# Kernel optimization log

Hardware: AMD Instinct MI355X
Metric: run time of the kernel (lower is better)

Reference implementation:

```python
import jax, jax.numpy as jnp
import numpy as np

NUMERICAL_STABILIZER = 1e-3


def relu_kernel(data, projection_matrix):
    # data: [B,L,H,D], projection_matrix: [M,D] -> [B,L,H,M]
    ratio = 1.0 / jnp.sqrt(jnp.asarray(projection_matrix.shape[0], dtype=data.dtype))
    data_dash = ratio * jnp.einsum('blhd,md->blhm', data, projection_matrix)
    return jax.nn.relu(data_dash) + NUMERICAL_STABILIZER


def favor_causal(query, key, value, projection_matrix):
    # query/key/value: [B,L,H,D]; projection_matrix: [M,D]
    qp = relu_kernel(query, projection_matrix)  # [B,L,H,M]
    kp = relu_kernel(key, projection_matrix)    # [B,L,H,M]
    # move L to scan axis: [L,B,H,*]
    qs = jnp.transpose(qp, (1, 0, 2, 3))
    ks = jnp.transpose(kp, (1, 0, 2, 3))
    vs = jnp.transpose(value, (1, 0, 2, 3))

    B, H, M = qs.shape[1], qs.shape[2], qs.shape[3]
    D = vs.shape[3]
    kv0 = jnp.zeros((B, H, M, D), dtype=qs.dtype)
    ksum0 = jnp.zeros((B, H, M), dtype=qs.dtype)

    def step(carry, inp):
        kv_sum, k_sum = carry
        q_t, k_t, v_t = inp  # [B,H,M], [B,H,M], [B,H,D]
        kv_sum = kv_sum + jnp.einsum('bhm,bhd->bhmd', k_t, v_t)
        k_sum = k_sum + k_t
        num_t = jnp.einsum('bhmd,bhm->bhd', kv_sum, q_t)  # [B,H,D]
        den_t = jnp.einsum('bhm,bhm->bh', q_t, k_sum)     # [B,H]
        return (kv_sum, k_sum), (num_t, den_t)

    _, (num, den) = jax.lax.scan(step, (kv0, ksum0), (qs, ks, vs))
    # num: [L,B,H,D], den: [L,B,H]
    out = num / den[..., None]
    return jnp.transpose(out, (1, 0, 2, 3))  # [B,L,H,D]


def setup_inputs() -> dict:
    key = jax.random.key(0)
    k1, k2, k3, k4 = jax.random.split(key, 4)
    B, L, H, D, M = 2, 4096, 8, 64, 128
    return {
        'query': jax.random.normal(k1, (B, L, H, D), dtype=jnp.float32),
        'key': jax.random.normal(k2, (B, L, H, D), dtype=jnp.float32),
        'value': jax.random.normal(k3, (B, L, H, D), dtype=jnp.float32),
        'projection_matrix': jax.random.normal(k4, (M, D), dtype=jnp.float32),
    }


def reference(query, key, value, projection_matrix):
    return favor_causal(query, key, value, projection_matrix)
```

## Files before the change

kernel.cpp:

```cpp
#include <hip/hip_runtime.h>


#define B_ 2
#define L_ 4096
#define H_ 8
#define D_ 64
#define M_ 128
#define BH_ 16
#define HD_ 512
#define LHD_ (L_*HD_)
#define C_ 64
#define T_ 64
#define RATIO 0.08838834764831845f
#define EPS 1e-3f

#define REC_CS 8320
#define REC_F  8192
#define QF_OFF 8519680
#define N2_OFF 16908288
#define RS_OFF 25296896
#define P_OFF  25427968

#define VT_S  72
#define KFT_S 72
#define TM_S  136

typedef __attribute__((ext_vector_type(8))) short bf16x8;
typedef __attribute__((ext_vector_type(4))) short bf16x4;
typedef __attribute__((ext_vector_type(4))) float f32x4;

__device__ __forceinline__ short f2bf(float f) {
  union { float f; unsigned u; } x; x.f = f;
  unsigned r = (x.u + 0x7fffu + ((x.u >> 16) & 1u)) >> 16;
  return (short)r;
}
__device__ __forceinline__ float bf2f(short s) {
  union { unsigned u; float f; } x; x.u = ((unsigned)(unsigned short)s) << 16;
  return x.f;
}
__device__ __forceinline__ bf16x8 load_cvt8(const float* p) {
  float4 a = *(const float4*)p;
  float4 b = *(const float4*)(p + 4);
  union { bf16x8 v; short s[8]; } u;
  u.s[0]=f2bf(a.x); u.s[1]=f2bf(a.y); u.s[2]=f2bf(a.z); u.s[3]=f2bf(a.w);
  u.s[4]=f2bf(b.x); u.s[5]=f2bf(b.y); u.s[6]=f2bf(b.z); u.s[7]=f2bf(b.w);
  return u.v;
}
#define MFMA(a,b,c) __builtin_amdgcn_mfma_f32_16x16x32_bf16((a),(b),(c),0,0,0)

__global__ __launch_bounds__(256) void k0(
    const float* __restrict__ P, unsigned short* __restrict__ ws)
{
  const int i = (blockIdx.x*256 + threadIdx.x)*4;
  float4 p4 = *(const float4*)(P + i);
  union { bf16x4 v; short s[4]; } u;
  u.s[0]=f2bf(p4.x); u.s[1]=f2bf(p4.y); u.s[2]=f2bf(p4.z); u.s[3]=f2bf(p4.w);
  *(bf16x4*)(ws + P_OFF + i) = u.v;
}

__global__ __launch_bounds__(256) void k1(
    const float* __restrict__ qq, const float* __restrict__ kk,
    const float* __restrict__ vv, unsigned short* __restrict__ ws)
{
  __shared__ short Vt[64*VT_S];
  __shared__ short Kft[128*KFT_S];
  __shared__ short KfTM[64*TM_S];
  __shared__ short QfTM[64*TM_S];

  const int tid = threadIdx.x, bid = blockIdx.x;
  const int bh = bid >> 6, c = bid & 63;
  const int b = bh >> 3, h = bh & 7;
  const int lane = tid & 63, w = tid >> 6, quad = lane >> 4, l15 = lane & 15;
  const size_t gbase = (size_t)b*LHD_ + (size_t)h*D_;
  const int t0 = c*T_;
  const unsigned short* Pb = ws + P_OFF;

  for (int fi = tid; fi < 64*16; fi += 256) {
    int t = fi >> 4, d4 = (fi & 15)*4;
    float4 v4 = *(const float4*)(vv + gbase + (size_t)(t0+t)*HD_ + d4);
    Vt[(d4+0)*VT_S + t] = f2bf(v4.x);
    Vt[(d4+1)*VT_S + t] = f2bf(v4.y);
    Vt[(d4+2)*VT_S + t] = f2bf(v4.z);
    Vt[(d4+3)*VT_S + t] = f2bf(v4.w);
  }

  const float* qrow = qq + gbase + (size_t)(t0 + 16*w + l15)*HD_;
  const float* krow = kk + gbase + (size_t)(t0 + 16*w + l15)*HD_;
  bf16x8 bq0 = load_cvt8(qrow + quad*8);
  bf16x8 bq1 = load_cvt8(qrow + 32 + quad*8);
  bf16x8 bk0 = load_cvt8(krow + quad*8);
  bf16x8 bk1 = load_cvt8(krow + 32 + quad*8);
  #pragma unroll
  for (int ct = 0; ct < 8; ++ct) {
    bf16x8 ap0 = *(const bf16x8*)(Pb + (ct*16 + l15)*64 + quad*8);
    bf16x8 ap1 = *(const bf16x8*)(Pb + (ct*16 + l15)*64 + 32 + quad*8);
    f32x4 qa = {0.f,0.f,0.f,0.f}, ka = {0.f,0.f,0.f,0.f};
    qa = MFMA(ap0,bq0,qa); qa = MFMA(ap1,bq1,qa);
    ka = MFMA(ap0,bk0,ka); ka = MFMA(ap1,bk1,ka);
    union { bf16x4 v; short s[4]; } pq, pk;
    #pragma unroll
    for (int reg = 0; reg < 4; ++reg) {
      int m = 16*ct + 4*quad + reg;
      short qv = f2bf(fmaxf(qa[reg]*RATIO, 0.f) + EPS);
      short kv = f2bf(fmaxf(ka[reg]*RATIO, 0.f) + EPS);
      pq.s[reg] = qv; pk.s[reg] = kv;
      Kft[m*KFT_S + 16*w + l15] = kv;
    }
    *(bf16x4*)&QfTM[(16*w+l15)*TM_S + 16*ct + 4*quad] = pq.v;
    *(bf16x4*)&KfTM[(16*w+l15)*TM_S + 16*ct + 4*quad] = pk.v;
  }
  __syncthreads();

  unsigned short* csb = ws + (size_t)(bh*C_+c)*REC_CS;
  unsigned short* qfb = ws + QF_OFF + (size_t)(bh*C_+c)*REC_F;

  {
    int tt = tid >> 4, mb = (tid & 15)*8;
    #pragma unroll
    for (int j = 0; j < 4; ++j) {
      bf16x8 v8 = *(const bf16x8*)&QfTM[(tt + 16*j)*TM_S + mb];
      *(bf16x8*)(qfb + (tt + 16*j)*128 + mb) = v8;
    }
  }
  bf16x8 qfr[4];
  #pragma unroll
  for (int ks2 = 0; ks2 < 4; ++ks2)
    qfr[ks2] = *(const bf16x8*)&QfTM[(16*w+l15)*TM_S + ks2*32 + quad*8];

  if (tid < 128) {
    float s = 0.f;
    #pragma unroll
    for (int i = 0; i < 8; ++i) {
      bf16x8 r = *(const bf16x8*)&Kft[tid*KFT_S + 8*i];
      #pragma unroll
      for (int j = 0; j < 8; ++j) s += bf2f(r[j]);
    }
    csb[64*128 + tid] = (unsigned short)f2bf(s);
  }

  {
    bf16x8 av0 = *(const bf16x8*)&Vt[(16*w + l15)*VT_S + quad*8];
    bf16x8 av1 = *(const bf16x8*)&Vt[(16*w + l15)*VT_S + 32 + quad*8];
    #pragma unroll
    for (int mt = 0; mt < 8; ++mt) {
      bf16x8 b0 = *(const bf16x8*)&Kft[(16*mt + l15)*KFT_S + quad*8];
      bf16x8 b1 = *(const bf16x8*)&Kft[(16*mt + l15)*KFT_S + 32 + quad*8];
      f32x4 acc = {0.f,0.f,0.f,0.f};
      acc = MFMA(b0, av0, acc);
      acc = MFMA(b1, av1, acc);
      union { bf16x4 v; short s[4]; } pc;
      #pragma unroll
      for (int reg = 0; reg < 4; ++reg) pc.s[reg] = f2bf(acc[reg]);
      *(bf16x4*)(csb + (16*w + l15)*128 + 16*mt + 4*quad) = pc.v;
    }
  }
  __syncthreads();

  short* Sm = QfTM;

  f32x4 sacc[4];
  #pragma unroll
  for (int jt = 0; jt < 4; ++jt) { f32x4 z = {0.f,0.f,0.f,0.f}; sacc[jt] = z; }
  #pragma unroll
  for (int ks2 = 0; ks2 < 4; ++ks2) {
    #pragma unroll
    for (int jt = 0; jt < 4; ++jt) {
      bf16x8 bb = *(const bf16x8*)&KfTM[(16*jt + l15)*TM_S + ks2*32 + quad*8];
      sacc[jt] = MFMA(qfr[ks2], bb, sacc[jt]);
    }
  }
  float rs[4] = {0.f,0.f,0.f,0.f};
  #pragma unroll
  for (int jt = 0; jt < 4; ++jt)
    #pragma unroll
    for (int reg = 0; reg < 4; ++reg) {
      int row = 16*w + 4*quad + reg;
      int j = l15 + 16*jt;
      float val = (j <= row) ? sacc[jt][reg] : 0.f;
      rs[reg] += val;
      Sm[row*TM_S + j] = f2bf(val);
    }
  #pragma unroll
  for (int reg = 0; reg < 4; ++reg) {
    rs[reg] += __shfl_xor(rs[reg], 1);
    rs[reg] += __shfl_xor(rs[reg], 2);
    rs[reg] += __shfl_xor(rs[reg], 4);
    rs[reg] += __shfl_xor(rs[reg], 8);
  }
  float* rsg = (float*)(ws + RS_OFF);
  if (l15 < 4) {
    float v = (l15==0) ? rs[0] : (l15==1) ? rs[1] : (l15==2) ? rs[2] : rs[3];
    rsg[bh*L_ + t0 + 16*w + 4*quad + l15] = v;
  }

  float* n2 = (float*)(ws + N2_OFF);
  f32x4 nacc[4];
  #pragma unroll
  for (int ct = 0; ct < 4; ++ct) { f32x4 z = {0.f,0.f,0.f,0.f}; nacc[ct] = z; }
  #pragma unroll
  for (int kss = 0; kss < 2; ++kss) {
    bf16x8 sb = *(const bf16x8*)&Sm[(16*w + l15)*TM_S + kss*32 + quad*8];
    #pragma unroll
    for (int ct = 0; ct < 4; ++ct) {
      bf16x8 a = *(const bf16x8*)&Vt[(16*ct + l15)*VT_S + kss*32 + quad*8];
      nacc[ct] = MFMA(a, sb, nacc[ct]);
    }
  }
  const int tg = t0 + 16*w + l15;
  #pragma unroll
  for (int ct = 0; ct < 4; ++ct) {
    float4 o;
    o.x = nacc[ct][0]; o.y = nacc[ct][1]; o.z = nacc[ct][2]; o.w = nacc[ct][3];
    *(float4*)(n2 + gbase + (size_t)tg*HD_ + 16*ct + 4*quad) = o;
  }
}

__global__ __launch_bounds__(256) void k2(unsigned short* __restrict__ ws)
{
  const int gid = blockIdx.x*256 + threadIdx.x;
  const int bh = gid / REC_CS, e = gid % REC_CS;
  unsigned short* base = ws + (size_t)bh*C_*REC_CS + e;
  short v[64];
  #pragma unroll
  for (int c2 = 0; c2 < 64; ++c2) v[c2] = (short)base[(size_t)c2*REC_CS];
  float run = 0.f;
  #pragma unroll
  for (int c2 = 0; c2 < 64; ++c2) {
    base[(size_t)c2*REC_CS] = (unsigned short)f2bf(run);
    run += bf2f(v[c2]);
  }
}

__global__ __launch_bounds__(256) void k3(
    const unsigned short* __restrict__ ws, float* __restrict__ out)
{
  const int tid = threadIdx.x, bid = blockIdx.x;
  const int bh = bid >> 6, c = bid & 63;
  const int b = bh >> 3, h = bh & 7;
  const int lane = tid & 63, w = tid >> 6, quad = lane >> 4, l15 = lane & 15;
  const size_t gbase = (size_t)b*LHD_ + (size_t)h*D_;
  const int t0 = c*T_;
  const unsigned short* csb = ws + (size_t)(bh*C_+c)*REC_CS;
  const unsigned short* qfb = ws + QF_OFF + (size_t)(bh*C_+c)*REC_F;
  const float* n2 = (const float*)(ws + N2_OFF);
  const float* rsg = (const float*)(ws + RS_OFF);

  const int tg = t0 + 16*w + l15;

  float4 nv[4];
  #pragma unroll
  for (int ct = 0; ct < 4; ++ct)
    nv[ct] = *(const float4*)(n2 + gbase + (size_t)tg*HD_ + 16*ct + 4*quad);
  float rsv = rsg[bh*L_ + tg];

  bf16x8 qfB[4], ksf[4];
  #pragma unroll
  for (int ks2 = 0; ks2 < 4; ++ks2) {
    qfB[ks2] = *(const bf16x8*)(qfb + (16*w + l15)*128 + ks2*32 + quad*8);
    ksf[ks2] = *(const bf16x8*)(csb + 64*128 + ks2*32 + quad*8);
  }
  float dp = 0.f;
  #pragma unroll
  for (int ks2 = 0; ks2 < 4; ++ks2)
    #pragma unroll
    for (int j = 0; j < 8; ++j) dp += bf2f(qfB[ks2][j]) * bf2f(ksf[ks2][j]);
  dp += __shfl_xor(dp, 16);
  dp += __shfl_xor(dp, 32);
  float inv = 1.f / (dp + rsv);

  f32x4 nacc[4];
  #pragma unroll
  for (int ct = 0; ct < 4; ++ct) { f32x4 z = {0.f,0.f,0.f,0.f}; nacc[ct] = z; }
  #pragma unroll
  for (int ks2 = 0; ks2 < 4; ++ks2) {
    #pragma unroll
    for (int ct = 0; ct < 4; ++ct) {
      bf16x8 a = *(const bf16x8*)(csb + (16*ct + l15)*128 + ks2*32 + quad*8);
      nacc[ct] = MFMA(a, qfB[ks2], nacc[ct]);
    }
  }
  #pragma unroll
  for (int ct = 0; ct < 4; ++ct) {
    float4 o;
    o.x = (nacc[ct][0] + nv[ct].x) * inv;
    o.y = (nacc[ct][1] + nv[ct].y) * inv;
    o.z = (nacc[ct][2] + nv[ct].z) * inv;
    o.w = (nacc[ct][3] + nv[ct].w) * inv;
    *(float4*)(out + gbase + (size_t)tg*HD_ + 16*ct + 4*quad) = o;
  }
}

extern "C" void kernel_launch(void* const* d_in, const int* in_sizes, int n_in,
                              void* d_out, int out_size, void* d_ws, size_t ws_size,
                              hipStream_t stream) {
  const float* q = (const float*)d_in[0];
  const float* k = (const float*)d_in[1];
  const float* v = (const float*)d_in[2];
  const float* P = (const float*)d_in[3];
  float* out = (float*)d_out;
  unsigned short* ws = (unsigned short*)d_ws;

  dim3 blk(256);
  k0<<<dim3(8), blk, 0, stream>>>(P, ws);
  k1<<<dim3(BH_*C_), blk, 0, stream>>>(q, k, v, ws);
  k2<<<dim3(520), blk, 0, stream>>>(ws);
  k3<<<dim3(BH_*C_), blk, 0, stream>>>(ws, out);
}
```

Baseline: 133.0 us.

## Swizzle LDS layouts, vectorize chunk scan, stage chunk state in LDS

```diff
diff --git a/kernel.cpp b/kernel.cpp
--- a/kernel.cpp
+++ b/kernel.cpp
@@ -21,9 +21,8 @@
 #define RS_OFF 25296896
 #define P_OFF  25427968
 
-#define VT_S  72
-#define KFT_S 72
-#define TM_S  136
+#define SWZ64(r,c)  ((r)*64  + ((c) ^ (((r)&7)*8)))
+#define SWZ128(r,c) ((r)*128 + ((c) ^ (((r)&15)*8)))
 
 typedef __attribute__((ext_vector_type(8))) short bf16x8;
 typedef __attribute__((ext_vector_type(4))) short bf16x4;
@@ -38,9 +37,7 @@
   union { unsigned u; float f; } x; x.u = ((unsigned)(unsigned short)s) << 16;
   return x.f;
 }
-__device__ __forceinline__ bf16x8 load_cvt8(const float* p) {
-  float4 a = *(const float4*)p;
-  float4 b = *(const float4*)(p + 4);
+__device__ __forceinline__ bf16x8 cvt8(float4 a, float4 b) {
   union { bf16x8 v; short s[8]; } u;
   u.s[0]=f2bf(a.x); u.s[1]=f2bf(a.y); u.s[2]=f2bf(a.z); u.s[3]=f2bf(a.w);
   u.s[4]=f2bf(b.x); u.s[5]=f2bf(b.y); u.s[6]=f2bf(b.z); u.s[7]=f2bf(b.w);
@@ -62,10 +59,10 @@
     const float* __restrict__ qq, const float* __restrict__ kk,
     const float* __restrict__ vv, unsigned short* __restrict__ ws)
 {
-  __shared__ short Vt[64*VT_S];
-  __shared__ short Kft[128*KFT_S];
-  __shared__ short KfTM[64*TM_S];
-  __shared__ short QfTM[64*TM_S];
+  __shared__ short Vt[64*64];
+  __shared__ short Kft[128*64];
+  __shared__ short KfTM[64*128];
+  __shared__ short Scr[64*64];
 
   const int tid = threadIdx.x, bid = blockIdx.x;
   const int bh = bid >> 6, c = bid & 63;
@@ -73,23 +70,36 @@
   const int lane = tid & 63, w = tid >> 6, quad = lane >> 4, l15 = lane & 15;
   const size_t gbase = (size_t)b*LHD_ + (size_t)h*D_;
   const int t0 = c*T_;
+  const int trow = 16*w + l15;
   const unsigned short* Pb = ws + P_OFF;
+
+  const float* qrow = qq + gbase + (size_t)(t0 + trow)*HD_;
+  const float* krow = kk + gbase + (size_t)(t0 + trow)*HD_;
+  float4 q4a = *(const float4*)(qrow + quad*8);
+  float4 q4b = *(const float4*)(qrow + quad*8 + 4);
+  float4 q4c = *(const float4*)(qrow + 32 + quad*8);
+  float4 q4d = *(const float4*)(qrow + 32 + quad*8 + 4);
+  float4 k4a = *(const float4*)(krow + quad*8);
+  float4 k4b = *(const float4*)(krow + quad*8 + 4);
+  float4 k4c = *(const float4*)(krow + 32 + quad*8);
+  float4 k4d = *(const float4*)(krow + 32 + quad*8 + 4);
 
   for (int fi = tid; fi < 64*16; fi += 256) {
     int t = fi >> 4, d4 = (fi & 15)*4;
     float4 v4 = *(const float4*)(vv + gbase + (size_t)(t0+t)*HD_ + d4);
-    Vt[(d4+0)*VT_S + t] = f2bf(v4.x);
-    Vt[(d4+1)*VT_S + t] = f2bf(v4.y);
-    Vt[(d4+2)*VT_S + t] = f2bf(v4.z);
-    Vt[(d4+3)*VT_S + t] = f2bf(v4.w);
-  }
-
-  const float* qrow = qq + gbase + (size_t)(t0 + 16*w + l15)*HD_;
-  const float* krow = kk + gbase + (size_t)(t0 + 16*w + l15)*HD_;
-  bf16x8 bq0 = load_cvt8(qrow + quad*8);
-  bf16x8 bq1 = load_cvt8(qrow + 32 + quad*8);
-  bf16x8 bk0 = load_cvt8(krow + quad*8);
-  bf16x8 bk1 = load_cvt8(krow + 32 + quad*8);
+    Vt[SWZ64(d4+0, t)] = f2bf(v4.x);
+    Vt[SWZ64(d4+1, t)] = f2bf(v4.y);
+    Vt[SWZ64(d4+2, t)] = f2bf(v4.z);
+    Vt[SWZ64(d4+3, t)] = f2bf(v4.w);
+  }
+
+  bf16x8 bq0 = cvt8(q4a, q4b), bq1 = cvt8(q4c, q4d);
+  bf16x8 bk0 = cvt8(k4a, k4b), bk1 = cvt8(k4c, k4d);
+
+  unsigned short* qfb = ws + QF_OFF + (size_t)(bh*C_+c)*REC_F;
+  unsigned short* csb = ws + (size_t)(bh*C_+c)*REC_CS;
+
+  bf16x4 qreg[8];
   #pragma unroll
   for (int ct = 0; ct < 8; ++ct) {
     bf16x8 ap0 = *(const bf16x8*)(Pb + (ct*16 + l15)*64 + quad*8);
@@ -104,34 +114,29 @@
       short qv = f2bf(fmaxf(qa[reg]*RATIO, 0.f) + EPS);
       short kv = f2bf(fmaxf(ka[reg]*RATIO, 0.f) + EPS);
       pq.s[reg] = qv; pk.s[reg] = kv;
-      Kft[m*KFT_S + 16*w + l15] = kv;
-    }
-    *(bf16x4*)&QfTM[(16*w+l15)*TM_S + 16*ct + 4*quad] = pq.v;
-    *(bf16x4*)&KfTM[(16*w+l15)*TM_S + 16*ct + 4*quad] = pk.v;
+      Kft[SWZ64(m, trow)] = kv;
+    }
+    qreg[ct] = pq.v;
+    *(bf16x4*)(qfb + trow*128 + 16*ct + 4*quad) = pq.v;
+    *(bf16x4*)&KfTM[SWZ128(trow, 16*ct + 4*quad)] = pk.v;
+  }
+
+  bf16x8 qfr[4];
+  #pragma unroll
+  for (int p = 0; p < 2; ++p) {
+    #pragma unroll
+    for (int ct2 = 0; ct2 < 4; ++ct2)
+      *(bf16x4*)&Scr[SWZ64(trow, 16*ct2 + 4*quad)] = qreg[4*p + ct2];
+    qfr[2*p+0] = *(const bf16x8*)&Scr[SWZ64(trow, 8*quad)];
+    qfr[2*p+1] = *(const bf16x8*)&Scr[SWZ64(trow, 32 + 8*quad)];
   }
   __syncthreads();
-
-  unsigned short* csb = ws + (size_t)(bh*C_+c)*REC_CS;
-  unsigned short* qfb = ws + QF_OFF + (size_t)(bh*C_+c)*REC_F;
-
-  {
-    int tt = tid >> 4, mb = (tid & 15)*8;
-    #pragma unroll
-    for (int j = 0; j < 4; ++j) {
-      bf16x8 v8 = *(const bf16x8*)&QfTM[(tt + 16*j)*TM_S + mb];
-      *(bf16x8*)(qfb + (tt + 16*j)*128 + mb) = v8;
-    }
-  }
-  bf16x8 qfr[4];
-  #pragma unroll
-  for (int ks2 = 0; ks2 < 4; ++ks2)
-    qfr[ks2] = *(const bf16x8*)&QfTM[(16*w+l15)*TM_S + ks2*32 + quad*8];
 
   if (tid < 128) {
     float s = 0.f;
     #pragma unroll
     for (int i = 0; i < 8; ++i) {
-      bf16x8 r = *(const bf16x8*)&Kft[tid*KFT_S + 8*i];
+      bf16x8 r = *(const bf16x8*)&Kft[SWZ64(tid, 8*i)];
       #pragma unroll
       for (int j = 0; j < 8; ++j) s += bf2f(r[j]);
     }
@@ -139,24 +144,21 @@
   }
 
   {
-    bf16x8 av0 = *(const bf16x8*)&Vt[(16*w + l15)*VT_S + quad*8];
-    bf16x8 av1 = *(const bf16x8*)&Vt[(16*w + l15)*VT_S + 32 + quad*8];
+    bf16x8 av0 = *(const bf16x8*)&Vt[SWZ64(trow, 8*quad)];
+    bf16x8 av1 = *(const bf16x8*)&Vt[SWZ64(trow, 32 + 8*quad)];
     #pragma unroll
     for (int mt = 0; mt < 8; ++mt) {
-      bf16x8 b0 = *(const bf16x8*)&Kft[(16*mt + l15)*KFT_S + quad*8];
-      bf16x8 b1 = *(const bf16x8*)&Kft[(16*mt + l15)*KFT_S + 32 + quad*8];
+      bf16x8 b0 = *(const bf16x8*)&Kft[SWZ64(16*mt + l15, 8*quad)];
+      bf16x8 b1 = *(const bf16x8*)&Kft[SWZ64(16*mt + l15, 32 + 8*quad)];
       f32x4 acc = {0.f,0.f,0.f,0.f};
       acc = MFMA(b0, av0, acc);
       acc = MFMA(b1, av1, acc);
       union { bf16x4 v; short s[4]; } pc;
       #pragma unroll
       for (int reg = 0; reg < 4; ++reg) pc.s[reg] = f2bf(acc[reg]);
-      *(bf16x4*)(csb + (16*w + l15)*128 + 16*mt + 4*quad) = pc.v;
-    }
-  }
-  __syncthreads();
-
-  short* Sm = QfTM;
+      *(bf16x4*)(csb + trow*128 + 16*mt + 4*quad) = pc.v;
+    }
+  }
 
   f32x4 sacc[4];
   #pragma unroll
@@ -165,10 +167,12 @@
   for (int ks2 = 0; ks2 < 4; ++ks2) {
     #pragma unroll
     for (int jt = 0; jt < 4; ++jt) {
-      bf16x8 bb = *(const bf16x8*)&KfTM[(16*jt + l15)*TM_S + ks2*32 + quad*8];
+      bf16x8 bb = *(const bf16x8*)&KfTM[SWZ128(16*jt + l15, 32*ks2 + 8*quad)];
       sacc[jt] = MFMA(qfr[ks2], bb, sacc[jt]);
     }
   }
+
+  short* Sm = Scr;
   float rs[4] = {0.f,0.f,0.f,0.f};
   #pragma unroll
   for (int jt = 0; jt < 4; ++jt)
@@ -178,7 +182,7 @@
       int j = l15 + 16*jt;
       float val = (j <= row) ? sacc[jt][reg] : 0.f;
       rs[reg] += val;
-      Sm[row*TM_S + j] = f2bf(val);
+      Sm[SWZ64(row, j)] = f2bf(val);
     }
   #pragma unroll
   for (int reg = 0; reg < 4; ++reg) {
@@ -199,14 +203,14 @@
   for (int ct = 0; ct < 4; ++ct) { f32x4 z = {0.f,0.f,0.f,0.f}; nacc[ct] = z; }
   #pragma unroll
   for (int kss = 0; kss < 2; ++kss) {
-    bf16x8 sb = *(const bf16x8*)&Sm[(16*w + l15)*TM_S + kss*32 + quad*8];
+    bf16x8 sb = *(const bf16x8*)&Sm[SWZ64(trow, 32*kss + 8*quad)];
     #pragma unroll
     for (int ct = 0; ct < 4; ++ct) {
-      bf16x8 a = *(const bf16x8*)&Vt[(16*ct + l15)*VT_S + kss*32 + quad*8];
+      bf16x8 a = *(const bf16x8*)&Vt[SWZ64(16*ct + l15, 32*kss + 8*quad)];
       nacc[ct] = MFMA(a, sb, nacc[ct]);
     }
   }
-  const int tg = t0 + 16*w + l15;
+  const int tg = t0 + trow;
   #pragma unroll
   for (int ct = 0; ct < 4; ++ct) {
     float4 o;
@@ -215,25 +219,30 @@
   }
 }
 
-__global__ __launch_bounds__(256) void k2(unsigned short* __restrict__ ws)
+__global__ __launch_bounds__(64) void k2(unsigned short* __restrict__ ws)
 {
-  const int gid = blockIdx.x*256 + threadIdx.x;
-  const int bh = gid / REC_CS, e = gid % REC_CS;
+  const int gid = blockIdx.x*64 + threadIdx.x;
+  const int bh = gid / 2080, e = (gid % 2080)*4;
   unsigned short* base = ws + (size_t)bh*C_*REC_CS + e;
-  short v[64];
-  #pragma unroll
-  for (int c2 = 0; c2 < 64; ++c2) v[c2] = (short)base[(size_t)c2*REC_CS];
-  float run = 0.f;
+  bf16x4 v[64];
+  #pragma unroll
+  for (int c2 = 0; c2 < 64; ++c2) v[c2] = *(const bf16x4*)(base + (size_t)c2*REC_CS);
+  float run[4] = {0.f,0.f,0.f,0.f};
   #pragma unroll
   for (int c2 = 0; c2 < 64; ++c2) {
-    base[(size_t)c2*REC_CS] = (unsigned short)f2bf(run);
-    run += bf2f(v[c2]);
+    union { bf16x4 v; short s[4]; } wv;
+    #pragma unroll
+    for (int j = 0; j < 4; ++j) { wv.s[j] = f2bf(run[j]); run[j] += bf2f(v[c2][j]); }
+    *(bf16x4*)(base + (size_t)c2*REC_CS) = wv.v;
   }
 }
 
 __global__ __launch_bounds__(256) void k3(
     const unsigned short* __restrict__ ws, float* __restrict__ out)
 {
+  __shared__ short csL[64*128];
+  __shared__ float ks_lds[128];
+
   const int tid = threadIdx.x, bid = blockIdx.x;
   const int bh = bid >> 6, c = bid & 63;
   const int b = bh >> 3, h = bh & 7;
@@ -244,26 +253,32 @@
   const unsigned short* qfb = ws + QF_OFF + (size_t)(bh*C_+c)*REC_F;
   const float* n2 = (const float*)(ws + N2_OFF);
   const float* rsg = (const float*)(ws + RS_OFF);
-
-  const int tg = t0 + 16*w + l15;
+  const int trow = 16*w + l15;
+  const int tg = t0 + trow;
+
+  for (int i = tid; i < 1024; i += 256) {
+    int row = i >> 4, cb = (i & 15)*8;
+    *(bf16x8*)&csL[SWZ128(row, cb)] = *(const bf16x8*)(csb + i*8);
+  }
+  if (tid < 128) ks_lds[tid] = bf2f((short)csb[64*128 + tid]);
 
   float4 nv[4];
   #pragma unroll
   for (int ct = 0; ct < 4; ++ct)
     nv[ct] = *(const float4*)(n2 + gbase + (size_t)tg*HD_ + 16*ct + 4*quad);
   float rsv = rsg[bh*L_ + tg];
-
-  bf16x8 qfB[4], ksf[4];
-  #pragma unroll
-  for (int ks2 = 0; ks2 < 4; ++ks2) {
-    qfB[ks2] = *(const bf16x8*)(qfb + (16*w + l15)*128 + ks2*32 + quad*8);
-    ksf[ks2] = *(const bf16x8*)(csb + 64*128 + ks2*32 + quad*8);
-  }
+  bf16x8 qfB[4];
+  #pragma unroll
+  for (int ks2 = 0; ks2 < 4; ++ks2)
+    qfB[ks2] = *(const bf16x8*)(qfb + trow*128 + ks2*32 + quad*8);
+
+  __syncthreads();
+
   float dp = 0.f;
   #pragma unroll
   for (int ks2 = 0; ks2 < 4; ++ks2)
     #pragma unroll
-    for (int j = 0; j < 8; ++j) dp += bf2f(qfB[ks2][j]) * bf2f(ksf[ks2][j]);
+    for (int j = 0; j < 8; ++j) dp += bf2f(qfB[ks2][j]) * ks_lds[ks2*32 + quad*8 + j];
   dp += __shfl_xor(dp, 16);
   dp += __shfl_xor(dp, 32);
   float inv = 1.f / (dp + rsv);
@@ -275,7 +290,7 @@
   for (int ks2 = 0; ks2 < 4; ++ks2) {
     #pragma unroll
     for (int ct = 0; ct < 4; ++ct) {
-      bf16x8 a = *(const bf16x8*)(csb + (16*ct + l15)*128 + ks2*32 + quad*8);
+      bf16x8 a = *(const bf16x8*)&csL[SWZ128(16*ct + l15, 32*ks2 + 8*quad)];
       nacc[ct] = MFMA(a, qfB[ks2], nacc[ct]);
     }
   }
@@ -300,9 +315,8 @@
   float* out = (float*)d_out;
   unsigned short* ws = (unsigned short*)d_ws;
 
-  dim3 blk(256);
-  k0<<<dim3(8), blk, 0, stream>>>(P, ws);
-  k1<<<dim3(BH_*C_), blk, 0, stream>>>(q, k, v, ws);
-  k2<<<dim3(520), blk, 0, stream>>>(ws);
-  k3<<<dim3(BH_*C_), blk, 0, stream>>>(ws, out);
-}
+  k0<<<dim3(8),      dim3(256), 0, stream>>>(P, ws);
+  k1<<<dim3(BH_*C_), dim3(256), 0, stream>>>(q, k, v, ws);
+  k2<<<dim3(520),    dim3(64),  0, stream>>>(ws);
+  k3<<<dim3(BH_*C_), dim3(256), 0, stream>>>(ws, out);
+}
```

Result: faster. 128.4 us (-3.5%).
